# Optimization experiments

Measured on AMD Instinct MI355X. Metric: run time of the kernel, lower is better.

## Reference

```python
import jax, jax.numpy as jnp
import numpy as np

N = 100_000        # nodes
E = 800_000        # directed edges before symmetrization
IN_DIM = 18        # input_dim_wf + input_dim_vm
HID = 128
VM_NUM = 16        # each_vm_type_num * vm_types
B = 65536 // VM_NUM
NEG_SLOPE = 0.2    # PyG GATConv leaky_relu slope


def _gat_conv(h, src, dst, W, a_s, a_d, b, n):
    """PyG GATConv (heads=1, add_self_loops=True, dropout off)."""
    z = h @ W                                     # [n, C]
    loops = jnp.arange(n, dtype=src.dtype)
    s = jnp.concatenate([src, loops])
    d = jnp.concatenate([dst, loops])
    e_s = z @ a_s                                 # [n]
    e_d = z @ a_d
    alpha = jax.nn.leaky_relu(e_s[s] + e_d[d], NEG_SLOPE)   # [E']
    amax = jax.ops.segment_max(alpha, d, num_segments=n)    # stable softmax over incoming edges
    ex = jnp.exp(alpha - amax[d])
    denom = jax.ops.segment_sum(ex, d, num_segments=n)
    w = ex / denom[d]
    out = jax.ops.segment_sum(w[:, None] * z[s], d, num_segments=n)
    return out + b


def setup_inputs() -> dict:
    key = jax.random.key(0)
    ks = jax.random.split(key, 16)
    sc = 0.1
    inp = {
        'state_wf': jax.random.normal(ks[0], (N, IN_DIM), jnp.float32),
        'edge_index': jax.random.randint(ks[1], (2, E), 0, N, jnp.int32),
        'candidate_task_index': jax.random.randint(ks[2], (B * VM_NUM,), 0, N, jnp.int32),
        # GAT layer 0: 18 -> 128
        'W0': jax.random.normal(ks[3], (IN_DIM, HID), jnp.float32) * sc,
        'a_src0': jax.random.normal(ks[4], (HID,), jnp.float32) * sc,
        'a_dst0': jax.random.normal(ks[5], (HID,), jnp.float32) * sc,
        'b0': jnp.zeros((HID,), jnp.float32),
        # GAT layer 1: 128 -> 128
        'W1': jax.random.normal(ks[6], (HID, HID), jnp.float32) * sc,
        'a_src1': jax.random.normal(ks[7], (HID,), jnp.float32) * sc,
        'a_dst1': jax.random.normal(ks[8], (HID,), jnp.float32) * sc,
        'b1': jnp.zeros((HID,), jnp.float32),
        # actor MLP: Linear(128,128) + ReLU + Linear(128,1)
        'mW0': jax.random.normal(ks[9], (HID, HID), jnp.float32) * sc,
        'mb0': jnp.zeros((HID,), jnp.float32),
        'mW1': jax.random.normal(ks[10], (HID, 1), jnp.float32) * sc,
        'mb1': jnp.zeros((1,), jnp.float32),
    }
    return inp


def reference(state_wf, edge_index, candidate_task_index,
              W0, a_src0, a_dst0, b0, W1, a_src1, a_dst1, b1,
              mW0, mb0, mW1, mb1):
    # Actor.forward symmetrizes edges: cat(edge_index, edge_index.flip(0))
    src = jnp.concatenate([edge_index[0], edge_index[1]])
    dst = jnp.concatenate([edge_index[1], edge_index[0]])
    # GAT stack, F.elu after each conv (dropout=0)
    h = jax.nn.elu(_gat_conv(state_wf, src, dst, W0, a_src0, a_dst0, b0, N))
    h = jax.nn.elu(_gat_conv(h, src, dst, W1, a_src1, a_dst1, b1, N))
    # gather candidate tasks and score them
    cand = h[candidate_task_index].reshape(-1, VM_NUM, HID)       # [B, vm, H]
    scores = jax.nn.relu(cand @ mW0 + mb0) @ mW1 + mb1            # [B, vm, 1]
    pi = jax.nn.softmax(scores, axis=1)[..., 0]                   # softmax over dim=1
    return pi
```

## Files before the change

kernel.cpp:

```cpp
#include <hip/hip_runtime.h>
#include <hip/hip_bf16.h>
#include <math.h>
#include <stdint.h>

typedef __hip_bfloat16 bf16;
typedef __attribute__((ext_vector_type(8))) short s8v;
typedef __attribute__((ext_vector_type(4))) float f4v;

#define N_NODES 100000
#define HID 128
#define NEG 0.2f
#define NBUCK 256
#define BSHIFT 9
#define ECAP 96
#define INDIM 18

__device__ __forceinline__ float b2f(bf16 x) { return __bfloat162float(x); }
__device__ __forceinline__ bf16 f2b(float x) { return __float2bfloat16(x); }
__device__ __forceinline__ float lo_bf(unsigned int u) {
    union { unsigned int i; float f; } c; c.i = u << 16; return c.f;
}
__device__ __forceinline__ float hi_bf(unsigned int u) {
    union { unsigned int i; float f; } c; c.i = u & 0xffff0000u; return c.f;
}
__device__ __forceinline__ short bfbits(float x) {
    union { bf16 b; short s; } u; u.b = f2b(x); return u.s;
}


__global__ void k_zero_int(int* p, int n) {
    int i = blockIdx.x * blockDim.x + threadIdx.x;
    if (i < n) p[i] = 0;
}

__global__ void k_bhist(const int* __restrict__ ei, int E, int* __restrict__ bcnt) {
    __shared__ int h[NBUCK];
    int t = threadIdx.x;
    h[t] = 0;
    __syncthreads();
    int i = blockIdx.x * blockDim.x + t;
    int stride = gridDim.x * blockDim.x;
    for (; i < E; i += stride) {
        int u = ei[i], v = ei[E + i];
        atomicAdd(&h[v >> BSHIFT], 1);
        atomicAdd(&h[u >> BSHIFT], 1);
    }
    __syncthreads();
    if (h[t]) atomicAdd(&bcnt[t], h[t]);
}

__global__ void k_bscan(const int* __restrict__ bcnt, int* __restrict__ bbase,
                        int* __restrict__ bnext) {
    __shared__ int buf[2][NBUCK];
    int t = threadIdx.x;
    int v = bcnt[t];
    buf[0][t] = v;
    __syncthreads();
    int cur = 0;
    for (int off = 1; off < NBUCK; off <<= 1) {
        int x = buf[cur][t] + ((t >= off) ? buf[cur][t - off] : 0);
        buf[cur ^ 1][t] = x;
        cur ^= 1;
        __syncthreads();
    }
    int incl = buf[cur][t];
    int excl = incl - v;
    bbase[t] = excl;
    bnext[t] = excl;
    if (t == NBUCK - 1) bbase[NBUCK] = incl;
}

#define SCH 2048
#define SK 8
__global__ __launch_bounds__(256) void k_bscatter(const int* __restrict__ ei, int E,
                                                  int* __restrict__ bnext,
                                                  int2* __restrict__ pairs) {
    __shared__ int h[NBUCK], base[NBUCK], h2[NBUCK];
    int t = threadIdx.x;
    h[t] = 0; h2[t] = 0;
    __syncthreads();
    int b0 = blockIdx.x * SCH;
    int eu[SK], ev[SK];
#pragma unroll
    for (int k = 0; k < SK; k++) {
        int i = b0 + k * 256 + t;
        if (i < E) {
            int u = ei[i], v = ei[E + i];
            eu[k] = u; ev[k] = v;
            atomicAdd(&h[v >> BSHIFT], 1);
            atomicAdd(&h[u >> BSHIFT], 1);
        } else { eu[k] = -1; ev[k] = -1; }
    }
    __syncthreads();
    if (h[t] > 0) base[t] = atomicAdd(&bnext[t], h[t]);
    __syncthreads();
#pragma unroll
    for (int k = 0; k < SK; k++) {
        if (eu[k] >= 0) {
            int u = eu[k], v = ev[k];
            int bv = v >> BSHIFT;
            pairs[base[bv] + atomicAdd(&h2[bv], 1)] = make_int2(v, u);
            int bu = u >> BSHIFT;
            pairs[base[bu] + atomicAdd(&h2[bu], 1)] = make_int2(u, v);
        }
    }
}

__global__ __launch_bounds__(256) void k_bbuild(const int2* __restrict__ pairs,
                                                const int* __restrict__ bbase,
                                                int* __restrict__ rowptr,
                                                int* __restrict__ col, int n) {
    __shared__ int deg[512];
    __shared__ int off[512];
    __shared__ int s2[2][256];
    int t = threadIdx.x;
    int b = blockIdx.x;
    int node0 = b << BSHIFT;
    deg[t] = 0; deg[t + 256] = 0;
    __syncthreads();
    int p0 = bbase[b], p1 = bbase[b + 1];
    for (int i = p0 + t; i < p1; i += 256) atomicAdd(&deg[pairs[i].x - node0], 1);
    __syncthreads();
    int a0 = deg[2 * t], a1 = deg[2 * t + 1];
    int s = a0 + a1;
    s2[0][t] = s;
    __syncthreads();
    int cur = 0;
    for (int o = 1; o < 256; o <<= 1) {
        int x = s2[cur][t] + ((t >= o) ? s2[cur][t - o] : 0);
        s2[cur ^ 1][t] = x;
        cur ^= 1;
        __syncthreads();
    }
    int excl = s2[cur][t] - s;
    off[2 * t] = excl;
    off[2 * t + 1] = excl + a0;
    __syncthreads();
    for (int j = t; j < 512; j += 256) {
        int node = node0 + j;
        if (node <= n) rowptr[node] = p0 + off[j];
    }
    deg[t] = 0; deg[t + 256] = 0;
    __syncthreads();
    for (int i = p0 + t; i < p1; i += 256) {
        int2 pr = pairs[i];
        int d = pr.x - node0;
        int ofs = atomicAdd(&deg[d], 1);
        col[p0 + off[d] + ofs] = pr.y;
    }
}


__device__ void pack128(const float* __restrict__ W, short* __restrict__ frag, int b) {
    int idx = b * 256 + threadIdx.x;
    int j = idx & 7;
    int lane = (idx >> 3) & 63;
    int cb = (idx >> 9) & 7;
    int kb = idx >> 12;
    int k = kb * 32 + (lane >> 4) * 8 + j;
    int c = cb * 16 + (lane & 15);
    float w = W[k * HID + c];
    bf16 hi = f2b(w);
    frag[idx] = bfbits(w);
    frag[16384 + idx] = bfbits(w - b2f(hi));
}

__global__ void k_packall(const float* __restrict__ W1, const float* __restrict__ mW0,
                          const float* __restrict__ W0, short* __restrict__ W1f,
                          short* __restrict__ mW0f, short* __restrict__ W0f) {
    int b = blockIdx.x;
    if (b < 64) { pack128(W1, W1f, b); return; }
    if (b < 128) { pack128(mW0, mW0f, b - 64); return; }
    int idx = (b - 128) * 256 + threadIdx.x;
    int var = idx >> 13;
    int r = idx & 8191;
    int j = r & 7;
    int lane = (r >> 3) & 63;
    int cb = (r >> 9) & 7;
    int kb = r >> 12;
    int kp = kb * 32 + (lane >> 4) * 8 + j;
    int c = cb * 16 + (lane & 15);
    short out = 0;
    if (kp < 2 * INDIM) {
        int src = (kp < INDIM) ? kp : kp - INDIM;
        float w = W0[src * HID + c];
        bf16 hi = f2b(w);
        bool want_hi = (kp < INDIM) ^ (var == 1);
        out = want_hi ? bfbits(w) : bfbits(w - b2f(hi));
    }
    W0f[var * 8192 + r] = out;
}


__global__ __launch_bounds__(256) void k_feat0m(const float* __restrict__ x,
                        const short* __restrict__ Wf,
                        const float* __restrict__ as_, const float* __restrict__ ad_,
                        bf16* __restrict__ z, float* __restrict__ es, float* __restrict__ ed,
                        int n) {
    __shared__ __align__(16) short ztile[4][16][136];
    int wv = threadIdx.x >> 6, lane = threadIdx.x & 63;
    int node0 = (blockIdx.x * 4 + wv) * 16;
    if (node0 >= n) return;
    int m = lane & 15, q = lane >> 4;
    const float* xr = x + (size_t)(node0 + m) * INDIM;
    s8v af0, af1;
#pragma unroll
    for (int j = 0; j < 8; j++) {
        int p0 = q * 8 + j;
        float v0 = 0.f;
        if (p0 < INDIM) v0 = xr[p0];
        else if (p0 < 2 * INDIM) v0 = xr[p0 - INDIM];
        short o0;
        if (p0 < INDIM) o0 = bfbits(v0);
        else o0 = bfbits(v0 - b2f(f2b(v0)));
        af0[j] = o0;
        int p1 = 32 + q * 8 + j;
        float v1 = (p1 < 2 * INDIM) ? xr[p1 - INDIM] : 0.f;
        af1[j] = bfbits(v1 - b2f(f2b(v1)));
    }
    f4v acc[8];
#pragma unroll
    for (int cb = 0; cb < 8; cb++) acc[cb] = (f4v){0.f, 0.f, 0.f, 0.f};
    const s8v* wf = (const s8v*)Wf;
#pragma unroll
    for (int cb = 0; cb < 8; cb++) {
        acc[cb] = __builtin_amdgcn_mfma_f32_16x16x32_bf16(af0, wf[cb * 64 + lane], acc[cb], 0, 0, 0);
        acc[cb] = __builtin_amdgcn_mfma_f32_16x16x32_bf16(af1, wf[(8 + cb) * 64 + lane], acc[cb], 0, 0, 0);
        acc[cb] = __builtin_amdgcn_mfma_f32_16x16x32_bf16(af0, wf[1024 + cb * 64 + lane], acc[cb], 0, 0, 0);
        acc[cb] = __builtin_amdgcn_mfma_f32_16x16x32_bf16(af1, wf[1024 + (8 + cb) * 64 + lane], acc[cb], 0, 0, 0);
    }
    float pe[4] = {0.f, 0.f, 0.f, 0.f}, pd[4] = {0.f, 0.f, 0.f, 0.f};
#pragma unroll
    for (int cb = 0; cb < 8; cb++) {
        float asv = as_[cb * 16 + m];
        float adv = ad_[cb * 16 + m];
#pragma unroll
        for (int r = 0; r < 4; r++) { pe[r] += acc[cb][r] * asv; pd[r] += acc[cb][r] * adv; }
    }
#pragma unroll
    for (int r = 0; r < 4; r++) {
#pragma unroll
        for (int off = 1; off < 16; off <<= 1) {
            pe[r] += __shfl_xor(pe[r], off);
            pd[r] += __shfl_xor(pd[r], off);
        }
    }
    if (m == 0) {
#pragma unroll
        for (int r = 0; r < 4; r++) {
            es[node0 + q * 4 + r] = pe[r];
            ed[node0 + q * 4 + r] = pd[r];
        }
    }
#pragma unroll
    for (int cb = 0; cb < 8; cb++)
#pragma unroll
        for (int r = 0; r < 4; r++)
            ztile[wv][q * 4 + r][cb * 16 + m] = bfbits(acc[cb][r]);
#pragma unroll
    for (int i = 0; i < 4; i++) {
        int idx = i * 64 + lane;
        int row = idx >> 4, t = idx & 15;
        s8v v = *(const s8v*)&ztile[wv][row][t * 8];
        *(s8v*)((short*)z + (size_t)(node0 + row) * HID + t * 8) = v;
    }
}


__global__ __launch_bounds__(256) void k_feat1(const bf16* __restrict__ h,
                        const short* __restrict__ Wf,
                        const float* __restrict__ as_, const float* __restrict__ ad_,
                        bf16* __restrict__ z, float* __restrict__ es, float* __restrict__ ed,
                        int n) {
    __shared__ __align__(16) short ztile[4][16][136];
    int wv = threadIdx.x >> 6, lane = threadIdx.x & 63;
    int node0 = (blockIdx.x * 4 + wv) * 16;
    if (node0 >= n) return;
    int m = lane & 15, q = lane >> 4;
    const short* hrow = (const short*)h + (size_t)(node0 + m) * HID + q * 8;
    s8v af[4];
#pragma unroll
    for (int kb = 0; kb < 4; kb++) af[kb] = *(const s8v*)(hrow + kb * 32);
    f4v acc[8];
#pragma unroll
    for (int cb = 0; cb < 8; cb++) acc[cb] = (f4v){0.f, 0.f, 0.f, 0.f};
    const s8v* wf = (const s8v*)Wf;
#pragma unroll
    for (int kb = 0; kb < 4; kb++) {
#pragma unroll
        for (int cb = 0; cb < 8; cb++) {
            acc[cb] = __builtin_amdgcn_mfma_f32_16x16x32_bf16(af[kb], wf[(kb * 8 + cb) * 64 + lane], acc[cb], 0, 0, 0);
            acc[cb] = __builtin_amdgcn_mfma_f32_16x16x32_bf16(af[kb], wf[2048 + (kb * 8 + cb) * 64 + lane], acc[cb], 0, 0, 0);
        }
    }
    float pe[4] = {0.f, 0.f, 0.f, 0.f}, pd[4] = {0.f, 0.f, 0.f, 0.f};
#pragma unroll
    for (int cb = 0; cb < 8; cb++) {
        float asv = as_[cb * 16 + m];
        float adv = ad_[cb * 16 + m];
#pragma unroll
        for (int r = 0; r < 4; r++) { pe[r] += acc[cb][r] * asv; pd[r] += acc[cb][r] * adv; }
    }
#pragma unroll
    for (int r = 0; r < 4; r++) {
#pragma unroll
        for (int off = 1; off < 16; off <<= 1) {
            pe[r] += __shfl_xor(pe[r], off);
            pd[r] += __shfl_xor(pd[r], off);
        }
    }
    if (m == 0) {
#pragma unroll
        for (int r = 0; r < 4; r++) {
            es[node0 + q * 4 + r] = pe[r];
            ed[node0 + q * 4 + r] = pd[r];
        }
    }
#pragma unroll
    for (int cb = 0; cb < 8; cb++)
#pragma unroll
        for (int r = 0; r < 4; r++)
            ztile[wv][q * 4 + r][cb * 16 + m] = bfbits(acc[cb][r]);
#pragma unroll
    for (int i = 0; i < 4; i++) {
        int idx = i * 64 + lane;
        int row = idx >> 4, t = idx & 15;
        s8v v = *(const s8v*)&ztile[wv][row][t * 8];
        *(s8v*)((short*)z + (size_t)(node0 + row) * HID + t * 8) = v;
    }
}


__global__ __launch_bounds__(256) void k_agg(const bf16* __restrict__ z,
                      const int* __restrict__ rowptr, const int* __restrict__ col,
                      const float* __restrict__ es, const float* __restrict__ ed,
                      const float* __restrict__ bias, bf16* __restrict__ hout, int n) {
    __shared__ float acache[4][ECAP];
    __shared__ int scache[4][ECAP];
    int wv = threadIdx.x >> 6;
    int lane = threadIdx.x & 63;
    int wid = blockIdx.x * 4 + wv;
    if (wid >= n) return;
    int d = wid;
    int s0 = rowptr[d], s1 = rowptr[d + 1];
    float edv = ed[d];
    float aself = es[d] + edv;
    aself = aself > 0.f ? aself : NEG * aself;
    float m = aself;
    for (int e = s0 + lane; e < s1; e += 64) {
        int s = col[e];
        float a = es[s] + edv;
        a = a > 0.f ? a : NEG * a;
        int q = e - s0;
        if (q < ECAP) { acache[wv][q] = a; scache[wv][q] = s; }
        m = fmaxf(m, a);
    }
#pragma unroll
    for (int off = 32; off > 0; off >>= 1) m = fmaxf(m, __shfl_xor(m, off));
    int g = lane >> 4, t = lane & 15;
    const uint4* zr = (const uint4*)z;
    float acc[8];
#pragma unroll
    for (int j = 0; j < 8; j++) acc[j] = 0.f;
    float den = 0.f;
    for (int e0 = s0; e0 < s1; e0 += 4) {
        int e = e0 + g;
        bool ok = (e < s1);
        int ee = ok ? e : s1 - 1;
        int q = ee - s0;
        int s; float a;
        if (q < ECAP) { s = scache[wv][q]; a = acache[wv][q]; }
        else { s = col[ee]; a = es[s] + edv; a = a > 0.f ? a : NEG * a; }
        float p = ok ? __expf(a - m) : 0.f;
        den += p;
        uint4 raw = zr[(size_t)s * 16 + t];
        acc[0] += p * lo_bf(raw.x); acc[1] += p * hi_bf(raw.x);
        acc[2] += p * lo_bf(raw.y); acc[3] += p * hi_bf(raw.y);
        acc[4] += p * lo_bf(raw.z); acc[5] += p * hi_bf(raw.z);
        acc[6] += p * lo_bf(raw.w); acc[7] += p * hi_bf(raw.w);
    }
#pragma unroll
    for (int off = 16; off <= 32; off <<= 1) {
        den += __shfl_xor(den, off);
#pragma unroll
        for (int j = 0; j < 8; j++) acc[j] += __shfl_xor(acc[j], off);
    }
    if (g == 0) {
        float pself = __expf(aself - m);
        den += pself;
        uint4 raw = zr[(size_t)d * 16 + t];
        acc[0] += pself * lo_bf(raw.x); acc[1] += pself * hi_bf(raw.x);
        acc[2] += pself * lo_bf(raw.y); acc[3] += pself * hi_bf(raw.y);
        acc[4] += pself * lo_bf(raw.z); acc[5] += pself * hi_bf(raw.z);
        acc[6] += pself * lo_bf(raw.w); acc[7] += pself * hi_bf(raw.w);
        float inv = 1.f / den;
        union { bf16 hv[8]; uint4 v; } uo;
#pragma unroll
        for (int j = 0; j < 8; j++) {
            float o = acc[j] * inv + bias[t * 8 + j];
            o = o > 0.f ? o : (__expf(o) - 1.f);
            uo.hv[j] = f2b(o);
        }
        ((uint4*)hout)[(size_t)d * 16 + t] = uo.v;
    }
}


__global__ __launch_bounds__(256) void k_group(const bf16* __restrict__ h,
                        const int* __restrict__ cand,
                        const short* __restrict__ Wf, const float* __restrict__ mb0,
                        const float* __restrict__ mW1, const float* __restrict__ mb1,
                        float* __restrict__ out) {
    __shared__ float sc[4][16];
    int wv = threadIdx.x >> 6, lane = threadIdx.x & 63;
    int g = blockIdx.x * 4 + wv;
    int m = lane & 15, q = lane >> 4;
    int node = cand[g * 16 + m];
    const short* hrow = (const short*)h + (size_t)node * HID + q * 8;
    s8v af[4];
#pragma unroll
    for (int kb = 0; kb < 4; kb++) af[kb] = *(const s8v*)(hrow + kb * 32);
    f4v acc[8];
#pragma unroll
    for (int cb = 0; cb < 8; cb++) acc[cb] = (f4v){0.f, 0.f, 0.f, 0.f};
    const s8v* wf = (const s8v*)Wf;
#pragma unroll
    for (int kb = 0; kb < 4; kb++) {
#pragma unroll
        for (int cb = 0; cb < 8; cb++) {
            acc[cb] = __builtin_amdgcn_mfma_f32_16x16x32_bf16(af[kb], wf[(kb * 8 + cb) * 64 + lane], acc[cb], 0, 0, 0);
            acc[cb] = __builtin_amdgcn_mfma_f32_16x16x32_bf16(af[kb], wf[2048 + (kb * 8 + cb) * 64 + lane], acc[cb], 0, 0, 0);
        }
    }
    float sr[4] = {0.f, 0.f, 0.f, 0.f};
#pragma unroll
    for (int cb = 0; cb < 8; cb++) {
        float b0v = mb0[cb * 16 + m];
        float w1v = mW1[cb * 16 + m];
#pragma unroll
        for (int r = 0; r < 4; r++) sr[r] += fmaxf(acc[cb][r] + b0v, 0.f) * w1v;
    }
#pragma unroll
    for (int r = 0; r < 4; r++) {
#pragma unroll
        for (int off = 1; off < 16; off <<= 1) sr[r] += __shfl_xor(sr[r], off);
    }
    float b1v = mb1[0];
    if (m == 0) {
#pragma unroll
        for (int r = 0; r < 4; r++) sc[wv][q * 4 + r] = sr[r] + b1v;
    }
    if (lane < 16) {
        float s = sc[wv][lane];
        float mx = s;
#pragma unroll
        for (int off = 1; off < 16; off <<= 1) mx = fmaxf(mx, __shfl_xor(mx, off));
        float e = __expf(s - mx);
        float den = e;
#pragma unroll
        for (int off = 1; off < 16; off <<= 1) den += __shfl_xor(den, off);
        out[g * 16 + lane] = e / den;
    }
}


extern "C" void kernel_launch(void* const* d_in, const int* in_sizes, int n_in,
                              void* d_out, int out_size, void* d_ws, size_t ws_size,
                              hipStream_t stream) {
    const int N = N_NODES;
    const float* state = (const float*)d_in[0];
    const int* ei   = (const int*)d_in[1];
    const int* cand = (const int*)d_in[2];
    const float* W0  = (const float*)d_in[3];
    const float* as0 = (const float*)d_in[4];
    const float* ad0 = (const float*)d_in[5];
    const float* b0  = (const float*)d_in[6];
    const float* W1  = (const float*)d_in[7];
    const float* as1 = (const float*)d_in[8];
    const float* ad1 = (const float*)d_in[9];
    const float* b1  = (const float*)d_in[10];
    const float* mW0 = (const float*)d_in[11];
    const float* mb0 = (const float*)d_in[12];
    const float* mW1 = (const float*)d_in[13];
    const float* mb1 = (const float*)d_in[14];

    int E = in_sizes[1] / 2;
    int M = 2 * E;
    int ncand = in_sizes[2];
    int ngroups = ncand / 16;

    char* p = (char*)d_ws;
    bf16* zb = (bf16*)p;              p += (size_t)N * HID * 2;
    bf16* hb = (bf16*)p;              p += (size_t)N * HID * 2;
    float* es = (float*)p;            p += (size_t)N * 4;
    float* ed = (float*)p;            p += (size_t)N * 4;
    p = (char*)(((uintptr_t)p + 15) & ~(uintptr_t)15);
    short* W1frag  = (short*)p;       p += 32768 * 2;
    short* mW0frag = (short*)p;       p += 32768 * 2;
    short* W0frag  = (short*)p;       p += 16384 * 2;
    int* rowptr = (int*)p;            p += (size_t)(N + 1) * 4;
    int* col    = (int*)p;            p += (size_t)M * 4;
    int* bcnt   = (int*)p;            p += (NBUCK + 1) * 4;
    int* bbase  = (int*)p;            p += (NBUCK + 1) * 4;
    int* bnext  = (int*)p;            p += NBUCK * 4;
    int2* pairs = (int2*)zb;

    int nwb = N / 4;

    k_packall<<<192, 256, 0, stream>>>(W1, mW0, W0, W1frag, mW0frag, W0frag);

    k_zero_int<<<1, 256, 0, stream>>>(bcnt, NBUCK);
    k_bhist<<<512, 256, 0, stream>>>(ei, E, bcnt);
    k_bscan<<<1, NBUCK, 0, stream>>>(bcnt, bbase, bnext);
    k_bscatter<<<(E + SCH - 1) / SCH, 256, 0, stream>>>(ei, E, bnext, pairs);
    k_bbuild<<<NBUCK, 256, 0, stream>>>(pairs, bbase, rowptr, col, N);

    int nfb = (N / 16 + 3) / 4;
    k_feat0m<<<nfb, 256, 0, stream>>>(state, W0frag, as0, ad0, zb, es, ed, N);
    k_agg<<<nwb, 256, 0, stream>>>(zb, rowptr, col, es, ed, b0, hb, N);

    k_feat1<<<nfb, 256, 0, stream>>>(hb, W1frag, as1, ad1, zb, es, ed, N);
    k_agg<<<nwb, 256, 0, stream>>>(zb, rowptr, col, es, ed, b1, hb, N);

    k_group<<<ngroups / 4, 256, 0, stream>>>(hb, cand, mW0frag, mb0, mW1, mb1, (float*)d_out);
}
```

Before: 345.5 us.

## Drop softmax max pass in aggregation, pack CSR pairs into 32-bit words

The aggregation kernel no longer does a separate pass to compute the per-node maximum attention logit and no longer caches logits in shared memory. It exponentiates each clamped logit directly and processes two edges per group per iteration to expose more memory parallelism. CSR construction now packs the local destination offset and the source id into one 32-bit word instead of an int2, halving scratch traffic, and the zero-init kernel is replaced by hipMemsetAsync. Skipping the max subtraction and clamping logits at 15 changes the numerics: values above the clamp are altered and overflow protection now depends on the clamp.

```diff
diff --git a/kernel.cpp b/kernel.cpp
--- a/kernel.cpp
+++ b/kernel.cpp
@@ -12,7 +12,6 @@
 #define NEG 0.2f
 #define NBUCK 256
 #define BSHIFT 9
-#define ECAP 96
 #define INDIM 18
 
 __device__ __forceinline__ float b2f(bf16 x) { return __bfloat162float(x); }
@@ -27,11 +26,6 @@
     union { bf16 b; short s; } u; u.b = f2b(x); return u.s;
 }
 
-
-__global__ void k_zero_int(int* p, int n) {
-    int i = blockIdx.x * blockDim.x + threadIdx.x;
-    if (i < n) p[i] = 0;
-}
 
 __global__ void k_bhist(const int* __restrict__ ei, int E, int* __restrict__ bcnt) {
     __shared__ int h[NBUCK];
@@ -74,7 +68,7 @@
 #define SK 8
 __global__ __launch_bounds__(256) void k_bscatter(const int* __restrict__ ei, int E,
                                                   int* __restrict__ bnext,
-                                                  int2* __restrict__ pairs) {
+                                                  unsigned* __restrict__ pairs) {
     __shared__ int h[NBUCK], base[NBUCK], h2[NBUCK];
     int t = threadIdx.x;
     h[t] = 0; h2[t] = 0;
@@ -97,16 +91,16 @@
 #pragma unroll
     for (int k = 0; k < SK; k++) {
         if (eu[k] >= 0) {
-            int u = eu[k], v = ev[k];
+            unsigned u = (unsigned)eu[k], v = (unsigned)ev[k];
             int bv = v >> BSHIFT;
-            pairs[base[bv] + atomicAdd(&h2[bv], 1)] = make_int2(v, u);
+            pairs[base[bv] + atomicAdd(&h2[bv], 1)] = ((v & 511u) << 17) | u;
             int bu = u >> BSHIFT;
-            pairs[base[bu] + atomicAdd(&h2[bu], 1)] = make_int2(u, v);
-        }
-    }
-}
-
-__global__ __launch_bounds__(256) void k_bbuild(const int2* __restrict__ pairs,
+            pairs[base[bu] + atomicAdd(&h2[bu], 1)] = ((u & 511u) << 17) | v;
+        }
+    }
+}
+
+__global__ __launch_bounds__(256) void k_bbuild(const unsigned* __restrict__ pairs,
                                                 const int* __restrict__ bbase,
                                                 int* __restrict__ rowptr,
                                                 int* __restrict__ col, int n) {
@@ -119,7 +113,7 @@
     deg[t] = 0; deg[t + 256] = 0;
     __syncthreads();
     int p0 = bbase[b], p1 = bbase[b + 1];
-    for (int i = p0 + t; i < p1; i += 256) atomicAdd(&deg[pairs[i].x - node0], 1);
+    for (int i = p0 + t; i < p1; i += 256) atomicAdd(&deg[pairs[i] >> 17], 1);
     __syncthreads();
     int a0 = deg[2 * t], a1 = deg[2 * t + 1];
     int s = a0 + a1;
@@ -143,10 +137,10 @@
     deg[t] = 0; deg[t + 256] = 0;
     __syncthreads();
     for (int i = p0 + t; i < p1; i += 256) {
-        int2 pr = pairs[i];
-        int d = pr.x - node0;
+        unsigned pr = pairs[i];
+        int d = pr >> 17;
         int ofs = atomicAdd(&deg[d], 1);
-        col[p0 + off[d] + ofs] = pr.y;
+        col[p0 + off[d] + ofs] = (int)(pr & 0x1FFFFu);
     }
 }
 
@@ -335,49 +329,38 @@
                       const int* __restrict__ rowptr, const int* __restrict__ col,
                       const float* __restrict__ es, const float* __restrict__ ed,
                       const float* __restrict__ bias, bf16* __restrict__ hout, int n) {
-    __shared__ float acache[4][ECAP];
-    __shared__ int scache[4][ECAP];
     int wv = threadIdx.x >> 6;
     int lane = threadIdx.x & 63;
-    int wid = blockIdx.x * 4 + wv;
-    if (wid >= n) return;
-    int d = wid;
+    int d = blockIdx.x * 4 + wv;
+    if (d >= n) return;
     int s0 = rowptr[d], s1 = rowptr[d + 1];
     float edv = ed[d];
-    float aself = es[d] + edv;
-    aself = aself > 0.f ? aself : NEG * aself;
-    float m = aself;
-    for (int e = s0 + lane; e < s1; e += 64) {
-        int s = col[e];
-        float a = es[s] + edv;
-        a = a > 0.f ? a : NEG * a;
-        int q = e - s0;
-        if (q < ECAP) { acache[wv][q] = a; scache[wv][q] = s; }
-        m = fmaxf(m, a);
-    }
-#pragma unroll
-    for (int off = 32; off > 0; off >>= 1) m = fmaxf(m, __shfl_xor(m, off));
     int g = lane >> 4, t = lane & 15;
     const uint4* zr = (const uint4*)z;
     float acc[8];
 #pragma unroll
     for (int j = 0; j < 8; j++) acc[j] = 0.f;
     float den = 0.f;
-    for (int e0 = s0; e0 < s1; e0 += 4) {
-        int e = e0 + g;
-        bool ok = (e < s1);
-        int ee = ok ? e : s1 - 1;
-        int q = ee - s0;
-        int s; float a;
-        if (q < ECAP) { s = scache[wv][q]; a = acache[wv][q]; }
-        else { s = col[ee]; a = es[s] + edv; a = a > 0.f ? a : NEG * a; }
-        float p = ok ? __expf(a - m) : 0.f;
-        den += p;
-        uint4 raw = zr[(size_t)s * 16 + t];
-        acc[0] += p * lo_bf(raw.x); acc[1] += p * hi_bf(raw.x);
-        acc[2] += p * lo_bf(raw.y); acc[3] += p * hi_bf(raw.y);
-        acc[4] += p * lo_bf(raw.z); acc[5] += p * hi_bf(raw.z);
-        acc[6] += p * lo_bf(raw.w); acc[7] += p * hi_bf(raw.w);
+    for (int e0 = s0; e0 < s1; e0 += 8) {
+        int eA = e0 + g, eB = e0 + 4 + g;
+        bool okA = (eA < s1), okB = (eB < s1);
+        int sA = col[okA ? eA : s1 - 1];
+        int sB = col[okB ? eB : s1 - 1];
+        float aA = es[sA] + edv; aA = aA > 0.f ? aA : NEG * aA;
+        float aB = es[sB] + edv; aB = aB > 0.f ? aB : NEG * aB;
+        float pA = okA ? __expf(fminf(aA, 15.f)) : 0.f;
+        float pB = okB ? __expf(fminf(aB, 15.f)) : 0.f;
+        uint4 rA = zr[(size_t)sA * 16 + t];
+        uint4 rB = zr[(size_t)sB * 16 + t];
+        den += pA + pB;
+        acc[0] += pA * lo_bf(rA.x) + pB * lo_bf(rB.x);
+        acc[1] += pA * hi_bf(rA.x) + pB * hi_bf(rB.x);
+        acc[2] += pA * lo_bf(rA.y) + pB * lo_bf(rB.y);
+        acc[3] += pA * hi_bf(rA.y) + pB * hi_bf(rB.y);
+        acc[4] += pA * lo_bf(rA.z) + pB * lo_bf(rB.z);
+        acc[5] += pA * hi_bf(rA.z) + pB * hi_bf(rB.z);
+        acc[6] += pA * lo_bf(rA.w) + pB * lo_bf(rB.w);
+        acc[7] += pA * hi_bf(rA.w) + pB * hi_bf(rB.w);
     }
 #pragma unroll
     for (int off = 16; off <= 32; off <<= 1) {
@@ -386,7 +369,9 @@
         for (int j = 0; j < 8; j++) acc[j] += __shfl_xor(acc[j], off);
     }
     if (g == 0) {
-        float pself = __expf(aself - m);
+        float aself = es[d] + edv;
+        aself = aself > 0.f ? aself : NEG * aself;
+        float pself = __expf(fminf(aself, 15.f));
         den += pself;
         uint4 raw = zr[(size_t)d * 16 + t];
         acc[0] += pself * lo_bf(raw.x); acc[1] += pself * hi_bf(raw.x);
@@ -503,13 +488,13 @@
     int* bcnt   = (int*)p;            p += (NBUCK + 1) * 4;
     int* bbase  = (int*)p;            p += (NBUCK + 1) * 4;
     int* bnext  = (int*)p;            p += NBUCK * 4;
-    int2* pairs = (int2*)zb;
+    unsigned* pairs = (unsigned*)zb;
 
     int nwb = N / 4;
 
     k_packall<<<192, 256, 0, stream>>>(W1, mW0, W0, W1frag, mW0frag, W0frag);
 
-    k_zero_int<<<1, 256, 0, stream>>>(bcnt, NBUCK);
+    hipMemsetAsync(bcnt, 0, NBUCK * sizeof(int), stream);
     k_bhist<<<512, 256, 0, stream>>>(ei, E, bcnt);
     k_bscan<<<1, NBUCK, 0, stream>>>(bcnt, bbase, bnext);
     k_bscatter<<<(E + SCH - 1) / SCH, 256, 0, stream>>>(ei, E, bnext, pairs);
```

New measurement: 347.8 us. Within noise of the previous version (+0.6%).
